# Performance work log

Measured on AMD Instinct MI355X. Metric: run time of the kernel, lower is better.

The kernel has to match this reference:

```python
import jax, jax.numpy as jnp
import numpy as np

N, D, E, T, R, KMEM, DE = 50000, 128, 800000, 400000, 1, 32, 16
EPS = 1e-5
BETA_MAX = 5.0
GRAD_CLIP = 1.0
STATE_CLIP = 10.0
STEP = 0.1
DAMP = 0.9999  # update_damping=1.0 clamped to 1-1e-4 as in __init__


def segment_logsumexp(s, idx, n):
    # numerically-stable per-segment logsumexp; empty segments contribute 0
    m = jax.ops.segment_max(s, idx, num_segments=n)
    ms = jnp.where(jnp.isfinite(m), m, 0.0)
    z = jax.ops.segment_sum(jnp.exp(s - ms[idx]), idx, num_segments=n)
    return jnp.where(z > 0, jnp.log(jnp.maximum(z, 1e-30)) + ms, 0.0)


def setup_inputs() -> dict:
    key = jax.random.key(0)
    ks = jax.random.split(key, 24)
    inv1 = jnp.log(jnp.expm1(jnp.float32(1.0)))  # _inv_softplus(1.0)
    xav = 0.5 * np.sqrt(2.0 / (2 * D))  # xavier_uniform gain=0.5 ~ std
    inp = {
        'X': jax.random.normal(ks[0], (N, D), jnp.float32),
        'edge_attr': jax.random.normal(ks[1], (E, DE), jnp.float32),
        'ln_gamma': jnp.ones((D,), jnp.float32),
        'ln_beta': jnp.zeros((D,), jnp.float32),
        'W_Q2': jax.random.normal(ks[2], (D, D), jnp.float32) * xav,
        'W_K2': jax.random.normal(ks[3], (D, D), jnp.float32) * xav,
        'W_Q3': jax.random.normal(ks[4], (D, R * D), jnp.float32) * xav,
        'W_K3': jax.random.normal(ks[5], (D, R * D), jnp.float32) * xav,
        'T_tau': jax.random.normal(ks[6], (2, R, D), jnp.float32) * 0.02,
        'W_Qm': jax.random.normal(ks[7], (D, D), jnp.float32) * xav,
        'W_Km': jax.random.normal(ks[8], (D, D), jnp.float32) * xav,
        'B_mem': jax.random.normal(ks[9], (KMEM, D), jnp.float32) / np.sqrt(D),
        'We1': jax.random.normal(ks[10], (DE, D), jnp.float32) / np.sqrt(DE),
        'be1': jnp.zeros((D,), jnp.float32),
        'We2': jax.random.normal(ks[11], (D, 1), jnp.float32) / np.sqrt(D),
        'be2': jnp.zeros((1,), jnp.float32),
        'lambda_2': inv1, 'lambda_3': inv1, 'lambda_m': inv1,
        'beta_2': inv1, 'beta_3': inv1, 'beta_m': inv1,
        'c_2': jax.random.randint(ks[12], (E,), 0, N),
        'u_2': jax.random.randint(ks[13], (E,), 0, N),
        'c_3': jax.random.randint(ks[14], (T,), 0, N),
        'u_3': jax.random.randint(ks[15], (T,), 0, N),
        'v_3': jax.random.randint(ks[16], (T,), 0, N),
        't_tau': jax.random.randint(ks[17], (T,), 0, 2),
    }
    return inp


def reference(X, edge_attr, ln_gamma, ln_beta, W_Q2, W_K2, W_Q3, W_K3, T_tau,
              W_Qm, W_Km, B_mem, We1, be1, We2, be2,
              lambda_2, lambda_3, lambda_m, beta_2, beta_3, beta_m,
              c_2, u_2, c_3, u_3, v_3, t_tau):
    sqrt_d = jnp.sqrt(jnp.float32(D))

    def energy(Xv):
        mu = jnp.mean(Xv, axis=-1, keepdims=True)
        var = jnp.var(Xv, axis=-1, keepdims=True)
        G = (Xv - mu) * jax.lax.rsqrt(var + EPS) * ln_gamma + ln_beta
        # pairwise (order-2) energy over edge list
        b2 = jnp.minimum(jax.nn.softplus(beta_2), BETA_MAX)
        Q2, K2 = G @ W_Q2, G @ W_K2
        a2 = (jax.nn.gelu(edge_attr @ We1 + be1) @ We2 + be2)[:, 0]  # edge_mlp bias
        s2 = b2 * (jnp.sum(Q2[c_2] * K2[u_2], axis=-1) / sqrt_d) + a2  # [E]
        E2 = -(jax.nn.softplus(lambda_2) / b2) * jnp.sum(segment_logsumexp(s2, c_2, N))
        # triplet (order-3) energy with per-type tensor T_tau
        b3 = jnp.minimum(jax.nn.softplus(beta_3), BETA_MAX)
        Q3 = (G @ W_Q3).reshape(-1, R, D)
        K3 = (G @ W_K3).reshape(-1, R, D)
        s3 = b3 * jnp.einsum('erd,erd,erd,erd->e', Q3[c_3], K3[u_3], K3[v_3],
                             T_tau[t_tau]) / jnp.float32(D)  # [T]
        E3 = -(jax.nn.softplus(lambda_3) / b3) * jnp.sum(segment_logsumexp(s3, c_3, N))
        # memory-bank energy
        bm = jnp.minimum(jax.nn.softplus(beta_m), BETA_MAX)
        sm = bm * ((G @ W_Qm) @ (B_mem @ W_Km).T) / sqrt_d  # [N,K]
        Em = -(jax.nn.softplus(lambda_m) / bm) * jnp.sum(jax.nn.logsumexp(sm, axis=1))
        return E2 + E3 + Em

    Eval, gX = jax.value_and_grad(energy)(X)
    gn = jnp.maximum(jnp.linalg.norm(gX, axis=-1, keepdims=True), 1e-6)
    gX = gX * jnp.minimum(GRAD_CLIP / gn, 1.0)
    X_next = X - STEP * DAMP * gX
    sn = jnp.maximum(jnp.linalg.norm(X_next, axis=-1, keepdims=True), 1e-6)
    X_next = X_next * jnp.minimum(STATE_CLIP / sn, 1.0)
    return (X_next, Eval)
```

## Files before the change

kernel.cpp:

```cpp
#include <hip/hip_runtime.h>

#define NN 50000
#define DD 128
#define EE 800000
#define TT 400000
#define KM 32
#define UU 320
#define SCAN_TILE 2048
#define SCAN_NB ((NN + SCAN_TILE - 1) / SCAN_TILE)

static constexpr float INV_SQRT_D = 0.08838834764831845f;
static constexpr float INV_D = 1.f / 128.f;

typedef __attribute__((ext_vector_type(8))) short bf16x8;
typedef __attribute__((ext_vector_type(4))) float f32x4;
typedef unsigned short ushort_t;

__device__ __forceinline__ float softplus_f(float x) {
  return (x > 20.f) ? x : log1pf(__expf(x));
}

__device__ __forceinline__ float gelu_fast(float x) {
  float p = fmaf(0.044715f * x * x, x, x);
  float e = __expf(-1.5957691216057308f * p);
  return x * __builtin_amdgcn_rcpf(1.f + e);
}

__device__ __forceinline__ float wredsum(float v) {
#pragma unroll
  for (int m = 32; m; m >>= 1) v += __shfl_xor(v, m, 64);
  return v;
}

__device__ __forceinline__ float redsum16(float v) {
#pragma unroll
  for (int m = 1; m < 16; m <<= 1) v += __shfl_xor(v, m, 64);
  return v;
}

__device__ __forceinline__ float blo(unsigned w) { return __uint_as_float(w << 16); }
__device__ __forceinline__ float bhi(unsigned w) { return __uint_as_float(w & 0xffff0000u); }
__device__ __forceinline__ unsigned pack_bf16(float a, float b) {
  unsigned ua = __float_as_uint(a); ua += 0x7fff + ((ua >> 16) & 1);
  unsigned ub = __float_as_uint(b); ub += 0x7fff + ((ub >> 16) & 1);
  return (ua >> 16) | (ub & 0xffff0000u);
}
__device__ __forceinline__ ushort_t bf16_1(float x) {
  unsigned u = __float_as_uint(x); u += 0x7fff + ((u >> 16) & 1);
  return (ushort_t)(u >> 16);
}
__device__ __forceinline__ void unp8(uint4 w, float* f) {
  f[0] = blo(w.x); f[1] = bhi(w.x); f[2] = blo(w.y); f[3] = bhi(w.y);
  f[4] = blo(w.z); f[5] = bhi(w.z); f[6] = blo(w.w); f[7] = bhi(w.w);
}
__device__ __forceinline__ uint4 pk8(const float* f) {
  uint4 r;
  r.x = pack_bf16(f[0], f[1]); r.y = pack_bf16(f[2], f[3]);
  r.z = pack_bf16(f[4], f[5]); r.w = pack_bf16(f[6], f[7]);
  return r;
}

__global__ void params_k(const float* l2, const float* l3, const float* lm,
                         const float* b2, const float* b3, const float* bm,
                         float* __restrict__ P) {
  if (threadIdx.x != 0) return;
  float B2 = fminf(softplus_f(b2[0]), 5.f);
  float B3 = fminf(softplus_f(b3[0]), 5.f);
  float Bm = fminf(softplus_f(bm[0]), 5.f);
  float S2 = softplus_f(l2[0]);
  float S3 = softplus_f(l3[0]);
  float Sm = softplus_f(lm[0]);
  P[0] = B2; P[1] = B3; P[2] = Bm;
  P[3] = -S2 * INV_SQRT_D; P[4] = -S3 * INV_D; P[5] = -Sm * INV_SQRT_D;
  P[6] = -S2 / B2; P[7] = -S3 / B3; P[8] = -Sm / Bm;
}

__global__ __launch_bounds__(256) void ln_fwd(const float* __restrict__ X,
                                              const float* __restrict__ gamma,
                                              const float* __restrict__ beta,
                                              unsigned* __restrict__ Gb,
                                              float* __restrict__ meanv,
                                              float* __restrict__ rstdv) {
  int row = blockIdx.x * 4 + (threadIdx.x >> 6);
  if (row >= NN) return;
  int l = threadIdx.x & 63;
  float2 x2 = *(const float2*)(X + row * DD + 2 * l);
  float mu = wredsum(x2.x + x2.y) * (1.f / DD);
  float d0 = x2.x - mu, d1 = x2.y - mu;
  float var = wredsum(d0 * d0 + d1 * d1) * (1.f / DD);
  float rstd = rsqrtf(var + 1e-5f);
  float2 g2 = *(const float2*)(gamma + 2 * l);
  float2 b2 = *(const float2*)(beta + 2 * l);
  float o0 = d0 * rstd * g2.x + b2.x;
  float o1 = d1 * rstd * g2.y + b2.y;
  Gb[(size_t)row * 64 + l] = pack_bf16(o0, o1);
  if (l == 0) { meanv[row] = mu; rstdv[row] = rstd; }
}

__global__ __launch_bounds__(256) void w_conv(const float* W0, const float* W1, const float* W2,
                                              const float* W3, const float* W4,
                                              ushort_t* __restrict__ Wt,
                                              ushort_t* __restrict__ Wc) {
  int idx = blockIdx.x * 256 + threadIdx.x;
  if (idx >= 640 * 128) return;
  const float* Ws[5] = {W0, W1, W2, W3, W4};
  int n = idx >> 7, k = idx & 127;
  Wt[idx] = bf16_1(Ws[n >> 7][(size_t)k * 128 + (n & 127)]);
  int k2 = idx >> 7, n2 = idx & 127;
  Wc[(size_t)n2 * 640 + k2] = bf16_1(Ws[k2 >> 7][(size_t)n2 * 128 + (k2 & 127)]);
}

__global__ __launch_bounds__(256) void mfma_fwd(const ushort_t* __restrict__ Gb,
                                                const ushort_t* __restrict__ Wt,
                                                ushort_t* __restrict__ QK, int M) {
  __shared__ ushort_t sB[64][136];
  int tid = threadIdx.x;
  int nb = blockIdx.y * 64;
  for (int idx = tid; idx < 64 * 16; idx += 256) {
    int r = idx >> 4, c8 = idx & 15;
    *(bf16x8*)&sB[r][c8 * 8] = *(const bf16x8*)(Wt + (size_t)(nb + r) * 128 + c8 * 8);
  }
  __syncthreads();
  int w = tid >> 6, l = tid & 63, quad = l >> 4, j = l & 15;
  int row0 = blockIdx.x * 64 + w * 16;
  int arow = row0 + j; if (arow >= M) arow = M - 1;
  const bf16x8* ap = (const bf16x8*)(Gb + (size_t)arow * 128);
  f32x4 acc[4];
#pragma unroll
  for (int nt = 0; nt < 4; nt++) acc[nt] = (f32x4){0.f, 0.f, 0.f, 0.f};
#pragma unroll
  for (int kc = 0; kc < 4; kc++) {
    bf16x8 a = ap[kc * 4 + quad];
#pragma unroll
    for (int nt = 0; nt < 4; nt++) {
      bf16x8 b = *(const bf16x8*)&sB[nt * 16 + j][kc * 32 + quad * 8];
      acc[nt] = __builtin_amdgcn_mfma_f32_16x16x32_bf16(a, b, acc[nt], 0, 0, 0);
    }
  }
#pragma unroll
  for (int nt = 0; nt < 4; nt++)
#pragma unroll
    for (int r = 0; r < 4; r++) {
      int row = row0 + quad * 4 + r;
      if (row < M) QK[(size_t)row * 640 + nb + nt * 16 + j] = bf16_1(acc[nt][r]);
    }
}

__global__ __launch_bounds__(256) void mfma_bwd(const ushort_t* __restrict__ dAll,
                                                const ushort_t* __restrict__ Wc,
                                                unsigned* __restrict__ dG, int M) {
  __shared__ ushort_t sB[64][40];
  int tid = threadIdx.x;
  int nb = blockIdx.y * 64;
  int w = tid >> 6, l = tid & 63, quad = l >> 4, j = l & 15;
  int row0 = blockIdx.x * 64 + w * 16;
  int arow = row0 + j; if (arow >= M) arow = M - 1;
  const ushort_t* arp = dAll + (size_t)arow * 640;
  f32x4 acc[4];
#pragma unroll
  for (int nt = 0; nt < 4; nt++) acc[nt] = (f32x4){0.f, 0.f, 0.f, 0.f};
  int sr = tid >> 2, sc = tid & 3;
  for (int kc = 0; kc < 20; kc++) {
    __syncthreads();
    *(bf16x8*)&sB[sr][sc * 8] = *(const bf16x8*)(Wc + (size_t)(nb + sr) * 640 + kc * 32 + sc * 8);
    __syncthreads();
    bf16x8 a = *(const bf16x8*)(arp + kc * 32 + quad * 8);
#pragma unroll
    for (int nt = 0; nt < 4; nt++) {
      bf16x8 b = *(const bf16x8*)&sB[nt * 16 + j][quad * 8];
      acc[nt] = __builtin_amdgcn_mfma_f32_16x16x32_bf16(a, b, acc[nt], 0, 0, 0);
    }
  }
#pragma unroll
  for (int nt = 0; nt < 4; nt++)
#pragma unroll
    for (int r = 0; r < 4; r++) {
      int row = row0 + quad * 4 + r;
      if (row < M) ((ushort_t*)dG)[(size_t)row * 128 + nb + nt * 16 + j] = bf16_1(acc[nt][r]);
    }
}

__global__ __launch_bounds__(256, 1) void gemm_km(const float* __restrict__ A,
                                                  const float* __restrict__ W,
                                                  float* __restrict__ C, int M) {
  __shared__ float As[32][132];
  __shared__ float Wst[128][136];
  const int tid = threadIdx.x;
  for (int idx = tid; idx < 128 * 128; idx += 256) {
    int k = idx >> 7, jj = idx & 127;
    Wst[k][jj] = W[k * 128 + jj];
  }
  for (int idx = tid; idx < 32 * 128; idx += 256) {
    int r = idx >> 7, d = idx & 127;
    As[r][d] = A[r * 128 + d];
  }
  __syncthreads();
  int r = tid >> 3, c0 = (tid & 7) * 16;
  float acc[16];
#pragma unroll
  for (int q = 0; q < 16; q++) acc[q] = 0.f;
  for (int k = 0; k < 128; k++) {
    float av = As[r][k];
#pragma unroll
    for (int q = 0; q < 16; q++) acc[q] = fmaf(av, Wst[k][c0 + q], acc[q]);
  }
#pragma unroll
  for (int q = 0; q < 16; q++) C[r * 128 + c0 + q] = acc[q];
}

__global__ __launch_bounds__(256) void edge_mlp(const float* __restrict__ EA,
                                                const float* __restrict__ We1,
                                                const float* __restrict__ be1,
                                                const float* __restrict__ We2,
                                                const float* __restrict__ be2,
                                                float* __restrict__ a2) {
  __shared__ float sW1[16 * 128];
  __shared__ float sb1[128];
  __shared__ float sW2[128];
  int tid = threadIdx.x;
  for (int i = tid; i < 2048; i += 256) sW1[i] = We1[i];
  if (tid < 128) { sb1[tid] = be1[tid]; sW2[tid] = We2[tid]; }
  __syncthreads();
  int w = tid >> 6, l = tid & 63;
  int m = l & 15, q = l >> 4;
  union u8 { bf16x8 v; ushort_t s[8]; };
  u8 bf[8];
  float bb[8], ww[8];
#pragma unroll
  for (int nt = 0; nt < 8; nt++) {
    int n = nt * 16 + m;
#pragma unroll
    for (int j = 0; j < 8; j++) {
      int k = q * 8 + j;
      bf[nt].s[j] = (k < 16) ? bf16_1(sW1[k * 128 + n]) : (ushort_t)0;
    }
    bb[nt] = sb1[n];
    ww[nt] = sW2[n];
  }
  float be2v = be2[0];
  for (int batch = 0; batch < 4; batch++) {
    int e0 = blockIdx.x * 256 + batch * 64 + w * 16;
    u8 af;
    if (q < 2) {
      const float* ep = EA + (size_t)(e0 + m) * 16 + q * 8;
      float4 v0 = *(const float4*)ep;
      float4 v1 = *(const float4*)(ep + 4);
      af.s[0] = bf16_1(v0.x); af.s[1] = bf16_1(v0.y);
      af.s[2] = bf16_1(v0.z); af.s[3] = bf16_1(v0.w);
      af.s[4] = bf16_1(v1.x); af.s[5] = bf16_1(v1.y);
      af.s[6] = bf16_1(v1.z); af.s[7] = bf16_1(v1.w);
    } else {
#pragma unroll
      for (int j = 0; j < 8; j++) af.s[j] = 0;
    }
    float s0 = 0.f, s1 = 0.f, s2 = 0.f, s3 = 0.f;
#pragma unroll
    for (int nt = 0; nt < 8; nt++) {
      float bias = bb[nt];
      f32x4 cin = (f32x4){bias, bias, bias, bias};
      f32x4 acc = __builtin_amdgcn_mfma_f32_16x16x32_bf16(af.v, bf[nt].v, cin, 0, 0, 0);
      float w2v = ww[nt];
      s0 = fmaf(gelu_fast(acc[0]), w2v, s0);
      s1 = fmaf(gelu_fast(acc[1]), w2v, s1);
      s2 = fmaf(gelu_fast(acc[2]), w2v, s2);
      s3 = fmaf(gelu_fast(acc[3]), w2v, s3);
    }
    s0 = redsum16(s0); s1 = redsum16(s1); s2 = redsum16(s2); s3 = redsum16(s3);
    if (m == 0) {
      int eb = e0 + q * 4;
      a2[eb + 0] = s0 + be2v;
      a2[eb + 1] = s1 + be2v;
      a2[eb + 2] = s2 + be2v;
      a2[eb + 3] = s3 + be2v;
    }
  }
}

__global__ __launch_bounds__(256) void hist2(const int* __restrict__ a,
                                             const int* __restrict__ b,
                                             int* __restrict__ ca,
                                             int* __restrict__ cb, int n) {
  int base = blockIdx.x * 2048 + threadIdx.x;
  if (base + 1792 < n) {
    int av[8], bv[8];
#pragma unroll
    for (int k = 0; k < 8; k++) { int e = base + k * 256; av[k] = a[e]; bv[k] = b[e]; }
#pragma unroll
    for (int k = 0; k < 8; k++) atomicAdd(&ca[av[k]], 1);
#pragma unroll
    for (int k = 0; k < 8; k++) atomicAdd(&cb[bv[k]], 1);
  } else {
#pragma unroll
    for (int k = 0; k < 8; k++) {
      int e = base + k * 256;
      if (e < n) { atomicAdd(&ca[a[e]], 1); atomicAdd(&cb[b[e]], 1); }
    }
  }
}

__global__ __launch_bounds__(256) void hist_t3(const int* __restrict__ c,
                                               const int* __restrict__ u,
                                               const int* __restrict__ v,
                                               int* __restrict__ cc,
                                               int* __restrict__ cuv, int n) {
  int base = blockIdx.x * 2048 + threadIdx.x;
  if (base + 1792 < n) {
    int cv[8], uv[8], vv[8];
#pragma unroll
    for (int k = 0; k < 8; k++) { int t = base + k * 256; cv[k] = c[t]; uv[k] = u[t]; vv[k] = v[t]; }
#pragma unroll
    for (int k = 0; k < 8; k++) atomicAdd(&cc[cv[k]], 1);
#pragma unroll
    for (int k = 0; k < 8; k++) atomicAdd(&cuv[uv[k]], 1);
#pragma unroll
    for (int k = 0; k < 8; k++) atomicAdd(&cuv[vv[k]], 1);
  } else {
#pragma unroll
    for (int k = 0; k < 8; k++) {
      int t = base + k * 256;
      if (t < n) { atomicAdd(&cc[c[t]], 1); atomicAdd(&cuv[u[t]], 1); atomicAdd(&cuv[v[t]], 1); }
    }
  }
}

__global__ __launch_bounds__(256) void scan_p1(const int* __restrict__ cnt,
                                               int* __restrict__ part) {
  int arr = blockIdx.y, b = blockIdx.x;
  const int* c = cnt + (size_t)arr * NN;
  int gi = b * SCAN_TILE + threadIdx.x * 8;
  int s = 0;
#pragma unroll
  for (int t = 0; t < 8; t++) s += (gi + t < NN) ? c[gi + t] : 0;
#pragma unroll
  for (int m = 32; m; m >>= 1) s += __shfl_xor(s, m, 64);
  __shared__ int wt[4];
  int lane = threadIdx.x & 63, wid = threadIdx.x >> 6;
  if (lane == 0) wt[wid] = s;
  __syncthreads();
  if (threadIdx.x == 0) part[arr * SCAN_NB + b] = wt[0] + wt[1] + wt[2] + wt[3];
}

__global__ __launch_bounds__(256) void scan_p2(int* __restrict__ part) {
  int w = threadIdx.x >> 6, l = threadIdx.x & 63;
  int v = (l < SCAN_NB) ? part[w * SCAN_NB + l] : 0;
  int x = v;
#pragma unroll
  for (int d = 1; d < 64; d <<= 1) {
    int y = __shfl_up(x, d, 64);
    if (l >= d) x += y;
  }
  if (l < SCAN_NB) part[w * SCAN_NB + l] = x - v;
}

__global__ __launch_bounds__(256) void scan_p3(const int* __restrict__ cnt,
                                               const int* __restrict__ part,
                                               int* __restrict__ rowptr,
                                               int* __restrict__ cursor) {
  int arr = blockIdx.y, b = blockIdx.x;
  const int* c = cnt + (size_t)arr * NN;
  int* rp = rowptr + (size_t)arr * (NN + 1);
  int* cur = cursor + (size_t)arr * NN;
  int tid = threadIdx.x;
  int gi = b * SCAN_TILE + tid * 8;
  int vals[8];
#pragma unroll
  for (int t = 0; t < 8; t++) vals[t] = (gi + t < NN) ? c[gi + t] : 0;
  int tsum = 0;
#pragma unroll
  for (int t = 0; t < 8; t++) tsum += vals[t];
  int lane = tid & 63, wid = tid >> 6;
  int x = tsum;
#pragma unroll
  for (int d = 1; d < 64; d <<= 1) {
    int y = __shfl_up(x, d, 64);
    if (lane >= d) x += y;
  }
  __shared__ int wt[4];
  if (lane == 63) wt[wid] = x;
  __syncthreads();
  int wadd = 0;
  for (int w = 0; w < wid; w++) wadd += wt[w];
  int running = part[arr * SCAN_NB + b] + wadd + x - tsum;
#pragma unroll
  for (int t = 0; t < 8; t++) {
    if (gi + t < NN) { rp[gi + t] = running; cur[gi + t] = running; }
    running += vals[t];
  }
  if (b == SCAN_NB - 1 && tid == 255) rp[NN] = running;
}

__global__ __launch_bounds__(256) void scat2(const int* __restrict__ c2,
                                             const int* __restrict__ u2,
                                             const float* __restrict__ a2,
                                             int* __restrict__ cuc,
                                             int* __restrict__ cuu,
                                             uint2* __restrict__ payc,
                                             uint2* __restrict__ payu, int n) {
  int base = blockIdx.x * 2048 + threadIdx.x;
  if (base + 1792 < n) {
    int c[8], u[8]; float a[8]; int p[8], p2[8];
#pragma unroll
    for (int k = 0; k < 8; k++) { int e = base + k * 256; c[k] = c2[e]; u[k] = u2[e]; a[k] = a2[e]; }
#pragma unroll
    for (int k = 0; k < 8; k++) p[k] = atomicAdd(&cuc[c[k]], 1);
#pragma unroll
    for (int k = 0; k < 8; k++) p2[k] = atomicAdd(&cuu[u[k]], 1);
#pragma unroll
    for (int k = 0; k < 8; k++) {
      uint2 t; t.x = (unsigned)u[k]; t.y = __float_as_uint(a[k]);
      payc[p[k]] = t;
    }
#pragma unroll
    for (int k = 0; k < 8; k++) {
      uint2 t; t.x = (unsigned)p[k]; t.y = (unsigned)c[k];
      payu[p2[k]] = t;
    }
  } else {
#pragma unroll
    for (int k = 0; k < 8; k++) {
      int e = base + k * 256;
      if (e < n) {
        int cc = c2[e], uu = u2[e];
        int pp = atomicAdd(&cuc[cc], 1);
        int qq = atomicAdd(&cuu[uu], 1);
        uint2 t; t.x = (unsigned)uu; t.y = __float_as_uint(a2[e]);
        payc[pp] = t;
        uint2 t2; t2.x = (unsigned)pp; t2.y = (unsigned)cc;
        payu[qq] = t2;
      }
    }
  }
}

__global__ __launch_bounds__(256) void scat_t3(const int* __restrict__ c3,
                                               const int* __restrict__ u3,
                                               const int* __restrict__ v3,
                                               const int* __restrict__ ttau,
                                               int* __restrict__ cuc,
                                               int* __restrict__ cuv,
                                               uint2* __restrict__ payc,
                                               uint2* __restrict__ payuv, int n) {
  int base = blockIdx.x * 1024 + threadIdx.x;
  if (base + 768 < n) {
    int c[4], u[4], v[4], ta[4]; int p[4], q1[4], q2[4];
#pragma unroll
    for (int k = 0; k < 4; k++) {
      int t = base + k * 256;
      c[k] = c3[t]; u[k] = u3[t]; v[k] = v3[t]; ta[k] = ttau[t] & 1;
    }
#pragma unroll
    for (int k = 0; k < 4; k++) p[k] = atomicAdd(&cuc[c[k]], 1);
#pragma unroll
    for (int k = 0; k < 4; k++) q1[k] = atomicAdd(&cuv[u[k]], 1);
#pragma unroll
    for (int k = 0; k < 4; k++) q2[k] = atomicAdd(&cuv[v[k]], 1);
#pragma unroll
    for (int k = 0; k < 4; k++) {
      uint2 a; a.x = ((unsigned)u[k] << 16) | (unsigned)v[k]; a.y = (unsigned)ta[k];
      payc[p[k]] = a;
    }
#pragma unroll
    for (int k = 0; k < 4; k++) {
      unsigned sp = ((unsigned)p[k] << 1) | (unsigned)ta[k];
      uint2 b1; b1.x = ((unsigned)v[k] << 16) | (unsigned)c[k]; b1.y = sp;
      payuv[q1[k]] = b1;
      uint2 b2; b2.x = ((unsigned)u[k] << 16) | (unsigned)c[k]; b2.y = sp;
      payuv[q2[k]] = b2;
    }
  } else {
#pragma unroll
    for (int k = 0; k < 4; k++) {
      int t = base + k * 256;
      if (t < n) {
        int c = c3[t], u = u3[t], v = v3[t], ta = ttau[t] & 1;
        int p = atomicAdd(&cuc[c], 1);
        int q1 = atomicAdd(&cuv[u], 1);
        int q2 = atomicAdd(&cuv[v], 1);
        unsigned sp = ((unsigned)p << 1) | (unsigned)ta;
        uint2 a; a.x = ((unsigned)u << 16) | (unsigned)v; a.y = (unsigned)ta;
        payc[p] = a;
        uint2 b1; b1.x = ((unsigned)v << 16) | (unsigned)c; b1.y = sp;
        payuv[q1] = b1;
        uint2 b2; b2.x = ((unsigned)u << 16) | (unsigned)c; b2.y = sp;
        payuv[q2] = b2;
      }
    }
  }
}

__global__ __launch_bounds__(256) void e2_fused(const unsigned* __restrict__ QK,
                                                const float* __restrict__ P,
                                                const uint2* __restrict__ pay,
                                                const int* __restrict__ rp,
                                                float* __restrict__ s2c,
                                                float* __restrict__ L2,
                                                unsigned* __restrict__ dAll) {
  int row = blockIdx.x * 4 + (threadIdx.x >> 6);
  if (row >= NN) return;
  int l = threadIdx.x & 63, g = l >> 4, j = l & 15;
  float b2s = P[0] * INV_SQRT_D, cw2 = P[3];
  float q[8];
  unp8(*(const uint4*)(QK + (size_t)row * UU + j * 4), q);
  int s = rp[row], e = rp[row + 1];
  float m = -3.0e38f, z = 0.f;
  float acc[8] = {0.f, 0.f, 0.f, 0.f, 0.f, 0.f, 0.f, 0.f};
  int i0 = s + g;
  uint4 kA = {0, 0, 0, 0}, kB = {0, 0, 0, 0};
  float aA = 0.f, aB = 0.f;
  if (i0 < e) {
    uint2 w = pay[i0]; aA = __uint_as_float(w.y);
    kA = *(const uint4*)(QK + (size_t)w.x * UU + 64 + j * 4);
  }
  if (i0 + 4 < e) {
    uint2 w = pay[i0 + 4]; aB = __uint_as_float(w.y);
    kB = *(const uint4*)(QK + (size_t)w.x * UU + 64 + j * 4);
  }
  for (int i = i0; i < e; i += 4) {
    uint4 kC = {0, 0, 0, 0}; float aC = 0.f;
    if (i + 8 < e) {
      uint2 w = pay[i + 8]; aC = __uint_as_float(w.y);
      kC = *(const uint4*)(QK + (size_t)w.x * UU + 64 + j * 4);
    }
    float k[8]; unp8(kA, k);
    float d = 0.f;
#pragma unroll
    for (int t = 0; t < 8; t++) d = fmaf(q[t], k[t], d);
    d = redsum16(d);
    float sv = b2s * d + aA;
    if (j == 0) s2c[i] = sv;
    if (sv <= m) {
      float p = __expf(sv - m);
      z += p;
#pragma unroll
      for (int t = 0; t < 8; t++) acc[t] = fmaf(p, k[t], acc[t]);
    } else {
      float r = __expf(m - sv);
      z = fmaf(z, r, 1.f);
#pragma unroll
      for (int t = 0; t < 8; t++) acc[t] = fmaf(acc[t], r, k[t]);
      m = sv;
    }
    kA = kB; aA = aB; kB = kC; aB = aC;
  }
  float mx = fmaxf(m, __shfl_xor(m, 16, 64));
  mx = fmaxf(mx, __shfl_xor(mx, 32, 64));
  float r = (z > 0.f) ? __expf(m - mx) : 0.f;
  float zz = z * r;
  zz += __shfl_xor(zz, 16, 64);
  zz += __shfl_xor(zz, 32, 64);
#pragma unroll
  for (int t = 0; t < 8; t++) {
    float v = acc[t] * r;
    v += __shfl_xor(v, 16, 64);
    v += __shfl_xor(v, 32, 64);
    acc[t] = v;
  }
  if (l == 0) L2[row] = (zz > 0.f) ? (mx + __logf(zz)) : 0.f;
  if (g == 0) {
    float coef = (zz > 0.f) ? cw2 / zz : 0.f;
    float o[8];
#pragma unroll
    for (int t = 0; t < 8; t++) o[t] = coef * acc[t];
    *(uint4*)(dAll + (size_t)row * UU + 0 + j * 4) = pk8(o);
  }
}

__global__ __launch_bounds__(256) void dk2_gather(const unsigned* __restrict__ QK,
                                                  const float* __restrict__ s2c,
                                                  const float* __restrict__ L2,
                                                  const float* __restrict__ P,
                                                  const uint2* __restrict__ pay,
                                                  const int* __restrict__ rp,
                                                  unsigned* __restrict__ dAll) {
  int row = blockIdx.x * 4 + (threadIdx.x >> 6);
  if (row >= NN) return;
  int l = threadIdx.x & 63, g = l >> 4, j = l & 15;
  float cw2 = P[3];
  int s = rp[row], e = rp[row + 1];
  float acc[8] = {0.f, 0.f, 0.f, 0.f, 0.f, 0.f, 0.f, 0.f};
  int i0 = s + g;
  uint4 qA = {0, 0, 0, 0}, qB = {0, 0, 0, 0};
  float scA = 0.f, lcA = 0.f, scB = 0.f, lcB = 0.f;
  if (i0 < e) {
    uint2 w = pay[i0]; scA = s2c[w.x]; lcA = L2[w.y];
    qA = *(const uint4*)(QK + (size_t)w.y * UU + 0 + j * 4);
  }
  if (i0 + 4 < e) {
    uint2 w = pay[i0 + 4]; scB = s2c[w.x]; lcB = L2[w.y];
    qB = *(const uint4*)(QK + (size_t)w.y * UU + 0 + j * 4);
  }
  for (int i = i0; i < e; i += 4) {
    uint4 qC = {0, 0, 0, 0}; float scC = 0.f, lcC = 0.f;
    if (i + 8 < e) {
      uint2 w = pay[i + 8]; scC = s2c[w.x]; lcC = L2[w.y];
      qC = *(const uint4*)(QK + (size_t)w.y * UU + 0 + j * 4);
    }
    float w = cw2 * __expf(scA - lcA);
    float qv[8]; unp8(qA, qv);
#pragma unroll
    for (int t = 0; t < 8; t++) acc[t] = fmaf(w, qv[t], acc[t]);
    qA = qB; scA = scB; lcA = lcB;
    qB = qC; scB = scC; lcB = lcC;
  }
#pragma unroll
  for (int t = 0; t < 8; t++) {
    float v = acc[t];
    v += __shfl_xor(v, 16, 64);
    v += __shfl_xor(v, 32, 64);
    acc[t] = v;
  }
  if (g == 0) *(uint4*)(dAll + (size_t)row * UU + 64 + j * 4) = pk8(acc);
}

__global__ __launch_bounds__(256) void t3_fused(const unsigned* __restrict__ QK,
                                                const float* __restrict__ Tt,
                                                const float* __restrict__ P,
                                                const uint2* __restrict__ pay,
                                                const int* __restrict__ rp,
                                                float* __restrict__ s3c,
                                                float* __restrict__ L3,
                                                unsigned* __restrict__ dAll) {
  __shared__ float sT[2 * DD];
  int tid = threadIdx.x;
  sT[tid] = Tt[tid];
  __syncthreads();
  int row = blockIdx.x * 4 + (tid >> 6);
  if (row >= NN) return;
  int l = tid & 63, g = l >> 4, j = l & 15;
  float b3s = P[1] * INV_D, cw3 = P[4];
  float q[8];
  unp8(*(const uint4*)(QK + (size_t)row * UU + 128 + j * 4), q);
  int s = rp[row], e = rp[row + 1];
  float m = -3.0e38f, z = 0.f;
  float acc[8] = {0.f, 0.f, 0.f, 0.f, 0.f, 0.f, 0.f, 0.f};
  int i0 = s + g;
  uint4 kuA = {0, 0, 0, 0}, kvA = {0, 0, 0, 0};
  uint4 kuB = {0, 0, 0, 0}, kvB = {0, 0, 0, 0};
  int taA = 0, taB = 0;
  if (i0 < e) {
    uint2 w = pay[i0]; int u = w.x >> 16, v = w.x & 0xffff; taA = (int)w.y;
    kuA = *(const uint4*)(QK + (size_t)u * UU + 192 + j * 4);
    kvA = *(const uint4*)(QK + (size_t)v * UU + 192 + j * 4);
  }
  if (i0 + 4 < e) {
    uint2 w = pay[i0 + 4]; int u = w.x >> 16, v = w.x & 0xffff; taB = (int)w.y;
    kuB = *(const uint4*)(QK + (size_t)u * UU + 192 + j * 4);
    kvB = *(const uint4*)(QK + (size_t)v * UU + 192 + j * 4);
  }
  for (int i = i0; i < e; i += 4) {
    uint4 kuC = {0, 0, 0, 0}, kvC = {0, 0, 0, 0}; int taC = 0;
    if (i + 8 < e) {
      uint2 w = pay[i + 8]; int u = w.x >> 16, v = w.x & 0xffff; taC = (int)w.y;
      kuC = *(const uint4*)(QK + (size_t)u * UU + 192 + j * 4);
      kvC = *(const uint4*)(QK + (size_t)v * UU + 192 + j * 4);
    }
    float ku[8], kv[8]; unp8(kuA, ku); unp8(kvA, kv);
    const float* tv = &sT[taA * DD + j * 8];
    float et[8], d = 0.f;
#pragma unroll
    for (int t = 0; t < 8; t++) { et[t] = ku[t] * kv[t] * tv[t]; d = fmaf(q[t], et[t], d); }
    d = redsum16(d);
    float sv = b3s * d;
    if (j == 0) s3c[i] = sv;
    if (sv <= m) {
      float p = __expf(sv - m);
      z += p;
#pragma unroll
      for (int t = 0; t < 8; t++) acc[t] = fmaf(p, et[t], acc[t]);
    } else {
      float r = __expf(m - sv);
      z = fmaf(z, r, 1.f);
#pragma unroll
      for (int t = 0; t < 8; t++) acc[t] = fmaf(acc[t], r, et[t]);
      m = sv;
    }
    kuA = kuB; kvA = kvB; taA = taB;
    kuB = kuC; kvB = kvC; taB = taC;
  }
  float mx = fmaxf(m, __shfl_xor(m, 16, 64));
  mx = fmaxf(mx, __shfl_xor(mx, 32, 64));
  float r = (z > 0.f) ? __expf(m - mx) : 0.f;
  float zz = z * r;
  zz += __shfl_xor(zz, 16, 64);
  zz += __shfl_xor(zz, 32, 64);
#pragma unroll
  for (int t = 0; t < 8; t++) {
    float v = acc[t] * r;
    v += __shfl_xor(v, 16, 64);
    v += __shfl_xor(v, 32, 64);
    acc[t] = v;
  }
  if (l == 0) L3[row] = (zz > 0.f) ? (mx + __logf(zz)) : 0.f;
  if (g == 0) {
    float coef = (zz > 0.f) ? cw3 / zz : 0.f;
    float o[8];
#pragma unroll
    for (int t = 0; t < 8; t++) o[t] = coef * acc[t];
    *(uint4*)(dAll + (size_t)row * UU + 128 + j * 4) = pk8(o);
  }
}

__global__ __launch_bounds__(256) void dk3_gather(const unsigned* __restrict__ QK,
                                                  const float* __restrict__ Tt,
                                                  const float* __restrict__ s3c,
                                                  const float* __restrict__ L3,
                                                  const float* __restrict__ P,
                                                  const uint2* __restrict__ pay,
                                                  const int* __restrict__ rp,
                                                  unsigned* __restrict__ dAll) {
  __shared__ float sT[2 * DD];
  int tid = threadIdx.x;
  sT[tid] = Tt[tid];
  __syncthreads();
  int row = blockIdx.x * 4 + (tid >> 6);
  if (row >= NN) return;
  int l = tid & 63, g = l >> 4, j = l & 15;
  float cw3 = P[4];
  int s = rp[row], e = rp[row + 1];
  float acc[8] = {0.f, 0.f, 0.f, 0.f, 0.f, 0.f, 0.f, 0.f};
  int i0 = s + g;
  uint4 qA = {0, 0, 0, 0}, kA = {0, 0, 0, 0};
  uint4 qB = {0, 0, 0, 0}, kB = {0, 0, 0, 0};
  int taA = 0, taB = 0;
  float scA = 0.f, lcA = 0.f, scB = 0.f, lcB = 0.f;
  if (i0 < e) {
    uint2 w = pay[i0]; int o = w.x >> 16, c = w.x & 0xffff; unsigned sp = w.y;
    taA = (int)(sp & 1); scA = s3c[sp >> 1]; lcA = L3[c];
    qA = *(const uint4*)(QK + (size_t)c * UU + 128 + j * 4);
    kA = *(const uint4*)(QK + (size_t)o * UU + 192 + j * 4);
  }
  if (i0 + 4 < e) {
    uint2 w = pay[i0 + 4]; int o = w.x >> 16, c = w.x & 0xffff; unsigned sp = w.y;
    taB = (int)(sp & 1); scB = s3c[sp >> 1]; lcB = L3[c];
    qB = *(const uint4*)(QK + (size_t)c * UU + 128 + j * 4);
    kB = *(const uint4*)(QK + (size_t)o * UU + 192 + j * 4);
  }
  for (int i = i0; i < e; i += 4) {
    uint4 qC = {0, 0, 0, 0}, kC = {0, 0, 0, 0}; int taC = 0;
    float scC = 0.f, lcC = 0.f;
    if (i + 8 < e) {
      uint2 w = pay[i + 8]; int o = w.x >> 16, c = w.x & 0xffff; unsigned sp = w.y;
      taC = (int)(sp & 1); scC = s3c[sp >> 1]; lcC = L3[c];
      qC = *(const uint4*)(QK + (size_t)c * UU + 128 + j * 4);
      kC = *(const uint4*)(QK + (size_t)o * UU + 192 + j * 4);
    }
    float w = cw3 * __expf(scA - lcA);
    float qv[8], ko[8]; unp8(qA, qv); unp8(kA, ko);
    const float* tv = &sT[taA * DD + j * 8];
#pragma unroll
    for (int t = 0; t < 8; t++) acc[t] = fmaf(w * tv[t], qv[t] * ko[t], acc[t]);
    qA = qB; kA = kB; taA = taB; scA = scB; lcA = lcB;
    qB = qC; kB = kC; taB = taC; scB = scC; lcB = lcC;
  }
#pragma unroll
  for (int t = 0; t < 8; t++) {
    float v = acc[t];
    v += __shfl_xor(v, 16, 64);
    v += __shfl_xor(v, 32, 64);
    acc[t] = v;
  }
  if (g == 0) *(uint4*)(dAll + (size_t)row * UU + 192 + j * 4) = pk8(acc);
}

__global__ __launch_bounds__(256) void em_row(const unsigned* __restrict__ QK,
                                              const float* __restrict__ Km,
                                              const float* __restrict__ P,
                                              unsigned* __restrict__ dAll,
                                              float* __restrict__ Lm) {
  __shared__ float sKm[KM * DD];
  int tid = threadIdx.x;
  for (int i = tid; i < KM * DD; i += 256) sKm[i] = Km[i];
  __syncthreads();
  int row = blockIdx.x * 4 + (tid >> 6);
  if (row >= NN) return;
  int l = tid & 63, g = l >> 4, j = l & 15;
  float bms = P[2] * INV_SQRT_D, cwm = P[5];
  float q[8];
  unp8(*(const uint4*)(QK + (size_t)row * UU + 256 + j * 4), q);
  float dk[8];
#pragma unroll
  for (int kk = 0; kk < 8; kk++) {
    int k = g * 8 + kk;
    const float* kr = &sKm[k * DD + j * 8];
    float d = 0.f;
#pragma unroll
    for (int t = 0; t < 8; t++) d = fmaf(q[t], kr[t], d);
    dk[kk] = redsum16(d) * bms;
  }
  float m = dk[0];
#pragma unroll
  for (int kk = 1; kk < 8; kk++) m = fmaxf(m, dk[kk]);
  float mx = fmaxf(m, __shfl_xor(m, 16, 64));
  mx = fmaxf(mx, __shfl_xor(mx, 32, 64));
  float p[8], z = 0.f;
#pragma unroll
  for (int kk = 0; kk < 8; kk++) { p[kk] = __expf(dk[kk] - mx); z += p[kk]; }
  float zz = z;
  zz += __shfl_xor(zz, 16, 64);
  zz += __shfl_xor(zz, 32, 64);
  if (l == 0) Lm[row] = mx + __logf(zz);
  float coef = cwm / zz;
  float acc[8] = {0.f, 0.f, 0.f, 0.f, 0.f, 0.f, 0.f, 0.f};
#pragma unroll
  for (int kk = 0; kk < 8; kk++) {
    int k = g * 8 + kk;
    const float* kr = &sKm[k * DD + j * 8];
    float pc_ = p[kk] * coef;
#pragma unroll
    for (int t = 0; t < 8; t++) acc[t] = fmaf(pc_, kr[t], acc[t]);
  }
#pragma unroll
  for (int t = 0; t < 8; t++) {
    float v = acc[t];
    v += __shfl_xor(v, 16, 64);
    v += __shfl_xor(v, 32, 64);
    acc[t] = v;
  }
  if (g == 0) *(uint4*)(dAll + (size_t)row * UU + 256 + j * 4) = pk8(acc);
}

__global__ __launch_bounds__(256) void ln_bwd(const float* __restrict__ X,
                                              const unsigned* __restrict__ dG,
                                              const float* __restrict__ gamma,
                                              const float* __restrict__ meanv,
                                              const float* __restrict__ rstdv,
                                              float* __restrict__ out) {
  int row = blockIdx.x * 4 + (threadIdx.x >> 6);
  if (row >= NN) return;
  int l = threadIdx.x & 63;
  float mu = meanv[row], rstd = rstdv[row];
  float2 x2 = *(const float2*)(X + row * DD + 2 * l);
  unsigned gw = dG[(size_t)row * 64 + l];
  float2 ga = *(const float2*)(gamma + 2 * l);
  float xh0 = (x2.x - mu) * rstd, xh1 = (x2.y - mu) * rstd;
  float dh0 = blo(gw) * ga.x, dh1 = bhi(gw) * ga.y;
  float sa = wredsum(dh0 + dh1) * (1.f / DD);
  float sb = wredsum(dh0 * xh0 + dh1 * xh1) * (1.f / DD);
  float dx0 = rstd * (dh0 - sa - xh0 * sb);
  float dx1 = rstd * (dh1 - sa - xh1 * sb);
  float gn = fmaxf(sqrtf(wredsum(dx0 * dx0 + dx1 * dx1)), 1e-6f);
  float sc = fminf(1.f / gn, 1.f);
  dx0 *= sc; dx1 *= sc;
  float xn0 = x2.x - 0.1f * 0.9999f * dx0;
  float xn1 = x2.y - 0.1f * 0.9999f * dx1;
  float sn = fmaxf(sqrtf(wredsum(xn0 * xn0 + xn1 * xn1)), 1e-6f);
  float sc2 = fminf(10.f / sn, 1.f);
  float2 o; o.x = xn0 * sc2; o.y = xn1 * sc2;
  *(float2*)(out + row * DD + 2 * l) = o;
}

__global__ __launch_bounds__(256) void eval_write(const float* __restrict__ L2,
                                                  const float* __restrict__ L3,
                                                  const float* __restrict__ Lm,
                                                  const float* __restrict__ P,
                                                  float* __restrict__ out) {
  int i = blockIdx.x * 256 + threadIdx.x;
  float a2 = 0.f, a3 = 0.f, am = 0.f;
  if (i < NN) { a2 = L2[i]; a3 = L3[i]; am = Lm[i]; }
  a2 = wredsum(a2); a3 = wredsum(a3); am = wredsum(am);
  __shared__ float r2[4], r3[4], rm[4];
  int wv = threadIdx.x >> 6, l = threadIdx.x & 63;
  if (l == 0) { r2[wv] = a2; r3[wv] = a3; rm[wv] = am; }
  __syncthreads();
  if (threadIdx.x == 0) {
    float S2 = r2[0] + r2[1] + r2[2] + r2[3];
    float S3 = r3[0] + r3[1] + r3[2] + r3[3];
    float Sm = rm[0] + rm[1] + rm[2] + rm[3];
    atomicAdd(out, P[6] * S2 + P[7] * S3 + P[8] * Sm);
  }
}

extern "C" void kernel_launch(void* const* d_in, const int* in_sizes, int n_in,
                              void* d_out, int out_size, void* d_ws, size_t ws_size,
                              hipStream_t stream) {
  (void)in_sizes; (void)n_in; (void)out_size;
  const float* X = (const float*)d_in[0];
  const float* EA = (const float*)d_in[1];
  const float* ln_g = (const float*)d_in[2];
  const float* ln_b = (const float*)d_in[3];
  const float* W_Q2 = (const float*)d_in[4];
  const float* W_K2 = (const float*)d_in[5];
  const float* W_Q3 = (const float*)d_in[6];
  const float* W_K3 = (const float*)d_in[7];
  const float* T_tau = (const float*)d_in[8];
  const float* W_Qm = (const float*)d_in[9];
  const float* W_Km = (const float*)d_in[10];
  const float* B_mem = (const float*)d_in[11];
  const float* We1 = (const float*)d_in[12];
  const float* be1 = (const float*)d_in[13];
  const float* We2 = (const float*)d_in[14];
  const float* be2 = (const float*)d_in[15];
  const float* l2s = (const float*)d_in[16];
  const float* l3s = (const float*)d_in[17];
  const float* lms = (const float*)d_in[18];
  const float* b2s = (const float*)d_in[19];
  const float* b3s = (const float*)d_in[20];
  const float* bms = (const float*)d_in[21];
  const int* c2 = (const int*)d_in[22];
  const int* u2 = (const int*)d_in[23];
  const int* c3 = (const int*)d_in[24];
  const int* u3 = (const int*)d_in[25];
  const int* v3 = (const int*)d_in[26];
  const int* ttau = (const int*)d_in[27];
  float* out = (float*)d_out;

  float* ws = (float*)d_ws;
  size_t off = 0;
  auto alloc = [&](size_t n) { float* p = ws + off; off += n; return p; };
  const size_t ND = (size_t)NN * DD;
  unsigned* Gb = (unsigned*)alloc(ND / 2);
  unsigned* QKall = (unsigned*)alloc((size_t)NN * UU);
  unsigned* dAll = (unsigned*)alloc((size_t)NN * UU);
  unsigned* dG = (unsigned*)alloc(ND / 2);
  ushort_t* Wt5 = (ushort_t*)alloc(640 * 128 / 2);
  ushort_t* Wcat = (ushort_t*)alloc(640 * 128 / 2);
  float* Km = alloc((size_t)KM * DD);
  float* a2 = alloc(EE);
  float* s2c = alloc(EE);
  float* s3c = alloc(TT);
  float* meanv = alloc(NN);
  float* rstdv = alloc(NN);
  float* L2 = alloc(NN);
  float* L3 = alloc(NN);
  float* Lm = alloc(NN);
  float* Pparams = alloc(16);
  int* cnt = (int*)alloc(4 * (size_t)NN);
  int* rowptr = (int*)alloc(4 * (size_t)(NN + 1));
  int* cursor = (int*)alloc(4 * (size_t)NN);
  int* spart = (int*)alloc(4 * SCAN_NB);
  uint2* payc2 = (uint2*)alloc(2 * (size_t)EE);
  uint2* payu2 = (uint2*)alloc(2 * (size_t)EE);
  uint2* payc3 = (uint2*)alloc(2 * (size_t)TT);
  uint2* payuv = (uint2*)alloc(4 * (size_t)TT);
  if (off * sizeof(float) > ws_size) return;

  int* cnt_c2 = cnt, *cnt_u2 = cnt + NN, *cnt_c3 = cnt + 2 * NN, *cnt_uv = cnt + 3 * NN;
  int* rp_c2 = rowptr, *rp_u2 = rowptr + (NN + 1), *rp_c3 = rowptr + 2 * (NN + 1), *rp_uv = rowptr + 3 * (NN + 1);
  int* cu_c2 = cursor, *cu_u2 = cursor + NN, *cu_c3 = cursor + 2 * NN, *cu_uv = cursor + 3 * NN;

  hipMemsetAsync(cnt, 0, 4ull * NN * sizeof(int), stream);
  hipMemsetAsync(out + ND, 0, sizeof(float), stream);

  params_k<<<1, 64, 0, stream>>>(l2s, l3s, lms, b2s, b3s, bms, Pparams);

  int rowB = (NN + 3) / 4;
  int mB = (NN + 63) / 64;

  ln_fwd<<<rowB, 256, 0, stream>>>(X, ln_g, ln_b, Gb, meanv, rstdv);
  w_conv<<<320, 256, 0, stream>>>(W_Q2, W_K2, W_Q3, W_K3, W_Qm, Wt5, Wcat);
  mfma_fwd<<<dim3(mB, 10), 256, 0, stream>>>((const ushort_t*)Gb, Wt5, (ushort_t*)QKall, NN);
  gemm_km<<<1, 256, 0, stream>>>(B_mem, W_Km, Km, KM);
  edge_mlp<<<EE / 256, 256, 0, stream>>>(EA, We1, be1, We2, be2, a2);

  hist2<<<(EE + 2047) / 2048, 256, 0, stream>>>(c2, u2, cnt_c2, cnt_u2, EE);
  hist_t3<<<(TT + 2047) / 2048, 256, 0, stream>>>(c3, u3, v3, cnt_c3, cnt_uv, TT);
  scan_p1<<<dim3(SCAN_NB, 4), 256, 0, stream>>>(cnt, spart);
  scan_p2<<<1, 256, 0, stream>>>(spart);
  scan_p3<<<dim3(SCAN_NB, 4), 256, 0, stream>>>(cnt, spart, rowptr, cursor);
  scat2<<<(EE + 2047) / 2048, 256, 0, stream>>>(c2, u2, a2, cu_c2, cu_u2, payc2, payu2, EE);
  scat_t3<<<(TT + 1023) / 1024, 256, 0, stream>>>(c3, u3, v3, ttau, cu_c3, cu_uv,
                                                  payc3, payuv, TT);

  e2_fused<<<rowB, 256, 0, stream>>>(QKall, Pparams, payc2, rp_c2, s2c, L2, dAll);
  dk2_gather<<<rowB, 256, 0, stream>>>(QKall, s2c, L2, Pparams, payu2, rp_u2, dAll);
  t3_fused<<<rowB, 256, 0, stream>>>(QKall, T_tau, Pparams, payc3, rp_c3, s3c, L3, dAll);
  dk3_gather<<<rowB, 256, 0, stream>>>(QKall, T_tau, s3c, L3, Pparams, payuv, rp_uv, dAll);
  em_row<<<rowB, 256, 0, stream>>>(QKall, Km, Pparams, dAll, Lm);

  mfma_bwd<<<dim3(mB, 2), 256, 0, stream>>>((const ushort_t*)dAll, Wcat, dG, NN);

  ln_bwd<<<rowB, 256, 0, stream>>>(X, dG, ln_g, meanv, rstdv, out);
  eval_write<<<(NN + 255) / 256, 256, 0, stream>>>(L2, L3, Lm, Pparams, out + ND);
}
```

Measured before the change: 861.6 us.

## Merge independent kernels into combined launches with block-range dispatch

Independent kernels are folded into single launches that split work by block index: the forward MFMA projection with the edge MLP, the two histograms, the two scatters, the e2/t3/memory-bank row kernels, and the two dk gathers. Histogram and scatter blocks now process 1024 elements instead of 2048, giving more blocks. The aim is to cut launch overhead and tail idle time by letting independent work overlap on the GPU. In exchange, shared memory is sized for the largest branch, register pressure is the maximum over branches, and blocks in one launch can be unevenly loaded.

```diff
diff --git a/kernel.cpp b/kernel.cpp
--- a/kernel.cpp
+++ b/kernel.cpp
@@ -6,6 +6,11 @@
 #define TT 400000
 #define KM 32
 #define UU 320
+#define ROWB 12500
+#define MB 782
+#define EDGE_BLKS 3125
+#define HB2 782
+#define HBT 391
 #define SCAN_TILE 2048
 #define SCAN_NB ((NN + SCAN_TILE - 1) / SCAN_TILE)
 
@@ -110,19 +115,19 @@
   Wc[(size_t)n2 * 640 + k2] = bf16_1(Ws[k2 >> 7][(size_t)n2 * 128 + (k2 & 127)]);
 }
 
-__global__ __launch_bounds__(256) void mfma_fwd(const ushort_t* __restrict__ Gb,
-                                                const ushort_t* __restrict__ Wt,
-                                                ushort_t* __restrict__ QK, int M) {
+__device__ void mfma_fwd_body(int bxr, int by, const ushort_t* __restrict__ Gb,
+                              const ushort_t* __restrict__ Wt,
+                              ushort_t* __restrict__ QK, int M) {
   __shared__ ushort_t sB[64][136];
   int tid = threadIdx.x;
-  int nb = blockIdx.y * 64;
+  int nb = by * 64;
   for (int idx = tid; idx < 64 * 16; idx += 256) {
     int r = idx >> 4, c8 = idx & 15;
     *(bf16x8*)&sB[r][c8 * 8] = *(const bf16x8*)(Wt + (size_t)(nb + r) * 128 + c8 * 8);
   }
   __syncthreads();
   int w = tid >> 6, l = tid & 63, quad = l >> 4, j = l & 15;
-  int row0 = blockIdx.x * 64 + w * 16;
+  int row0 = bxr * 64 + w * 16;
   int arow = row0 + j; if (arow >= M) arow = M - 1;
   const bf16x8* ap = (const bf16x8*)(Gb + (size_t)arow * 128);
   f32x4 acc[4];
@@ -146,74 +151,12 @@
     }
 }
 
-__global__ __launch_bounds__(256) void mfma_bwd(const ushort_t* __restrict__ dAll,
-                                                const ushort_t* __restrict__ Wc,
-                                                unsigned* __restrict__ dG, int M) {
-  __shared__ ushort_t sB[64][40];
-  int tid = threadIdx.x;
-  int nb = blockIdx.y * 64;
-  int w = tid >> 6, l = tid & 63, quad = l >> 4, j = l & 15;
-  int row0 = blockIdx.x * 64 + w * 16;
-  int arow = row0 + j; if (arow >= M) arow = M - 1;
-  const ushort_t* arp = dAll + (size_t)arow * 640;
-  f32x4 acc[4];
-#pragma unroll
-  for (int nt = 0; nt < 4; nt++) acc[nt] = (f32x4){0.f, 0.f, 0.f, 0.f};
-  int sr = tid >> 2, sc = tid & 3;
-  for (int kc = 0; kc < 20; kc++) {
-    __syncthreads();
-    *(bf16x8*)&sB[sr][sc * 8] = *(const bf16x8*)(Wc + (size_t)(nb + sr) * 640 + kc * 32 + sc * 8);
-    __syncthreads();
-    bf16x8 a = *(const bf16x8*)(arp + kc * 32 + quad * 8);
-#pragma unroll
-    for (int nt = 0; nt < 4; nt++) {
-      bf16x8 b = *(const bf16x8*)&sB[nt * 16 + j][quad * 8];
-      acc[nt] = __builtin_amdgcn_mfma_f32_16x16x32_bf16(a, b, acc[nt], 0, 0, 0);
-    }
-  }
-#pragma unroll
-  for (int nt = 0; nt < 4; nt++)
-#pragma unroll
-    for (int r = 0; r < 4; r++) {
-      int row = row0 + quad * 4 + r;
-      if (row < M) ((ushort_t*)dG)[(size_t)row * 128 + nb + nt * 16 + j] = bf16_1(acc[nt][r]);
-    }
-}
-
-__global__ __launch_bounds__(256, 1) void gemm_km(const float* __restrict__ A,
-                                                  const float* __restrict__ W,
-                                                  float* __restrict__ C, int M) {
-  __shared__ float As[32][132];
-  __shared__ float Wst[128][136];
-  const int tid = threadIdx.x;
-  for (int idx = tid; idx < 128 * 128; idx += 256) {
-    int k = idx >> 7, jj = idx & 127;
-    Wst[k][jj] = W[k * 128 + jj];
-  }
-  for (int idx = tid; idx < 32 * 128; idx += 256) {
-    int r = idx >> 7, d = idx & 127;
-    As[r][d] = A[r * 128 + d];
-  }
-  __syncthreads();
-  int r = tid >> 3, c0 = (tid & 7) * 16;
-  float acc[16];
-#pragma unroll
-  for (int q = 0; q < 16; q++) acc[q] = 0.f;
-  for (int k = 0; k < 128; k++) {
-    float av = As[r][k];
-#pragma unroll
-    for (int q = 0; q < 16; q++) acc[q] = fmaf(av, Wst[k][c0 + q], acc[q]);
-  }
-#pragma unroll
-  for (int q = 0; q < 16; q++) C[r * 128 + c0 + q] = acc[q];
-}
-
-__global__ __launch_bounds__(256) void edge_mlp(const float* __restrict__ EA,
-                                                const float* __restrict__ We1,
-                                                const float* __restrict__ be1,
-                                                const float* __restrict__ We2,
-                                                const float* __restrict__ be2,
-                                                float* __restrict__ a2) {
+__device__ void edge_mlp_body(int bx, const float* __restrict__ EA,
+                              const float* __restrict__ We1,
+                              const float* __restrict__ be1,
+                              const float* __restrict__ We2,
+                              const float* __restrict__ be2,
+                              float* __restrict__ a2) {
   __shared__ float sW1[16 * 128];
   __shared__ float sb1[128];
   __shared__ float sW2[128];
@@ -239,7 +182,7 @@
   }
   float be2v = be2[0];
   for (int batch = 0; batch < 4; batch++) {
-    int e0 = blockIdx.x * 256 + batch * 64 + w * 16;
+    int e0 = bx * 256 + batch * 64 + w * 16;
     u8 af;
     if (q < 2) {
       const float* ep = EA + (size_t)(e0 + m) * 16 + q * 8;
@@ -276,51 +219,142 @@
   }
 }
 
-__global__ __launch_bounds__(256) void hist2(const int* __restrict__ a,
-                                             const int* __restrict__ b,
-                                             int* __restrict__ ca,
-                                             int* __restrict__ cb, int n) {
-  int base = blockIdx.x * 2048 + threadIdx.x;
-  if (base + 1792 < n) {
-    int av[8], bv[8];
-#pragma unroll
-    for (int k = 0; k < 8; k++) { int e = base + k * 256; av[k] = a[e]; bv[k] = b[e]; }
-#pragma unroll
-    for (int k = 0; k < 8; k++) atomicAdd(&ca[av[k]], 1);
-#pragma unroll
-    for (int k = 0; k < 8; k++) atomicAdd(&cb[bv[k]], 1);
+__global__ __launch_bounds__(256) void fwd_k(const ushort_t* __restrict__ Gb,
+                                             const ushort_t* __restrict__ Wt,
+                                             ushort_t* __restrict__ QK,
+                                             const float* __restrict__ EA,
+                                             const float* __restrict__ We1,
+                                             const float* __restrict__ be1,
+                                             const float* __restrict__ We2,
+                                             const float* __restrict__ be2,
+                                             float* __restrict__ a2) {
+  int bx = blockIdx.x;
+  if (bx < MB * 10) {
+    mfma_fwd_body(bx / 10, bx % 10, Gb, Wt, QK, NN);
   } else {
-#pragma unroll
-    for (int k = 0; k < 8; k++) {
+    edge_mlp_body(bx - MB * 10, EA, We1, be1, We2, be2, a2);
+  }
+}
+
+__global__ __launch_bounds__(256) void mfma_bwd(const ushort_t* __restrict__ dAll,
+                                                const ushort_t* __restrict__ Wc,
+                                                unsigned* __restrict__ dG, int M) {
+  __shared__ ushort_t sB[64][40];
+  int tid = threadIdx.x;
+  int nb = blockIdx.y * 64;
+  int w = tid >> 6, l = tid & 63, quad = l >> 4, j = l & 15;
+  int row0 = blockIdx.x * 64 + w * 16;
+  int arow = row0 + j; if (arow >= M) arow = M - 1;
+  const ushort_t* arp = dAll + (size_t)arow * 640;
+  f32x4 acc[4];
+#pragma unroll
+  for (int nt = 0; nt < 4; nt++) acc[nt] = (f32x4){0.f, 0.f, 0.f, 0.f};
+  int sr = tid >> 2, sc = tid & 3;
+  for (int kc = 0; kc < 20; kc++) {
+    __syncthreads();
+    *(bf16x8*)&sB[sr][sc * 8] = *(const bf16x8*)(Wc + (size_t)(nb + sr) * 640 + kc * 32 + sc * 8);
+    __syncthreads();
+    bf16x8 a = *(const bf16x8*)(arp + kc * 32 + quad * 8);
+#pragma unroll
+    for (int nt = 0; nt < 4; nt++) {
+      bf16x8 b = *(const bf16x8*)&sB[nt * 16 + j][quad * 8];
+      acc[nt] = __builtin_amdgcn_mfma_f32_16x16x32_bf16(a, b, acc[nt], 0, 0, 0);
+    }
+  }
+#pragma unroll
+  for (int nt = 0; nt < 4; nt++)
+#pragma unroll
+    for (int r = 0; r < 4; r++) {
+      int row = row0 + quad * 4 + r;
+      if (row < M) ((ushort_t*)dG)[(size_t)row * 128 + nb + nt * 16 + j] = bf16_1(acc[nt][r]);
+    }
+}
+
+__global__ __launch_bounds__(256, 1) void gemm_km(const float* __restrict__ A,
+                                                  const float* __restrict__ W,
+                                                  float* __restrict__ C, int M) {
+  __shared__ float As[32][132];
+  __shared__ float Wst[128][136];
+  const int tid = threadIdx.x;
+  for (int idx = tid; idx < 128 * 128; idx += 256) {
+    int k = idx >> 7, jj = idx & 127;
+    Wst[k][jj] = W[k * 128 + jj];
+  }
+  for (int idx = tid; idx < 32 * 128; idx += 256) {
+    int r = idx >> 7, d = idx & 127;
+    As[r][d] = A[r * 128 + d];
+  }
+  __syncthreads();
+  int r = tid >> 3, c0 = (tid & 7) * 16;
+  float acc[16];
+#pragma unroll
+  for (int q = 0; q < 16; q++) acc[q] = 0.f;
+  for (int k = 0; k < 128; k++) {
+    float av = As[r][k];
+#pragma unroll
+    for (int q = 0; q < 16; q++) acc[q] = fmaf(av, Wst[k][c0 + q], acc[q]);
+  }
+#pragma unroll
+  for (int q = 0; q < 16; q++) C[r * 128 + c0 + q] = acc[q];
+}
+
+__device__ void hist2_body(int bx, const int* __restrict__ a,
+                           const int* __restrict__ b,
+                           int* __restrict__ ca, int* __restrict__ cb, int n) {
+  int base = bx * 1024 + threadIdx.x;
+  if (base + 768 < n) {
+    int av[4], bv[4];
+#pragma unroll
+    for (int k = 0; k < 4; k++) { int e = base + k * 256; av[k] = a[e]; bv[k] = b[e]; }
+#pragma unroll
+    for (int k = 0; k < 4; k++) atomicAdd(&ca[av[k]], 1);
+#pragma unroll
+    for (int k = 0; k < 4; k++) atomicAdd(&cb[bv[k]], 1);
+  } else {
+#pragma unroll
+    for (int k = 0; k < 4; k++) {
       int e = base + k * 256;
       if (e < n) { atomicAdd(&ca[a[e]], 1); atomicAdd(&cb[b[e]], 1); }
     }
   }
 }
 
-__global__ __launch_bounds__(256) void hist_t3(const int* __restrict__ c,
-                                               const int* __restrict__ u,
-                                               const int* __restrict__ v,
-                                               int* __restrict__ cc,
-                                               int* __restrict__ cuv, int n) {
-  int base = blockIdx.x * 2048 + threadIdx.x;
-  if (base + 1792 < n) {
-    int cv[8], uv[8], vv[8];
-#pragma unroll
-    for (int k = 0; k < 8; k++) { int t = base + k * 256; cv[k] = c[t]; uv[k] = u[t]; vv[k] = v[t]; }
-#pragma unroll
-    for (int k = 0; k < 8; k++) atomicAdd(&cc[cv[k]], 1);
-#pragma unroll
-    for (int k = 0; k < 8; k++) atomicAdd(&cuv[uv[k]], 1);
-#pragma unroll
-    for (int k = 0; k < 8; k++) atomicAdd(&cuv[vv[k]], 1);
+__device__ void hist_t3_body(int bx, const int* __restrict__ c,
+                             const int* __restrict__ u,
+                             const int* __restrict__ v,
+                             int* __restrict__ cc, int* __restrict__ cuv, int n) {
+  int base = bx * 1024 + threadIdx.x;
+  if (base + 768 < n) {
+    int cv[4], uv[4], vv[4];
+#pragma unroll
+    for (int k = 0; k < 4; k++) { int t = base + k * 256; cv[k] = c[t]; uv[k] = u[t]; vv[k] = v[t]; }
+#pragma unroll
+    for (int k = 0; k < 4; k++) atomicAdd(&cc[cv[k]], 1);
+#pragma unroll
+    for (int k = 0; k < 4; k++) atomicAdd(&cuv[uv[k]], 1);
+#pragma unroll
+    for (int k = 0; k < 4; k++) atomicAdd(&cuv[vv[k]], 1);
   } else {
 #pragma unroll
-    for (int k = 0; k < 8; k++) {
+    for (int k = 0; k < 4; k++) {
       int t = base + k * 256;
       if (t < n) { atomicAdd(&cc[c[t]], 1); atomicAdd(&cuv[u[t]], 1); atomicAdd(&cuv[v[t]], 1); }
     }
   }
+}
+
+__global__ __launch_bounds__(256) void hist_k(const int* __restrict__ c2,
+                                              const int* __restrict__ u2,
+                                              const int* __restrict__ c3,
+                                              const int* __restrict__ u3,
+                                              const int* __restrict__ v3,
+                                              int* __restrict__ cnt_c2,
+                                              int* __restrict__ cnt_u2,
+                                              int* __restrict__ cnt_c3,
+                                              int* __restrict__ cnt_uv) {
+  int bx = blockIdx.x;
+  if (bx < HB2) hist2_body(bx, c2, u2, cnt_c2, cnt_u2, EE);
+  else hist_t3_body(bx - HB2, c3, u3, v3, cnt_c3, cnt_uv, TT);
 }
 
 __global__ __launch_bounds__(256) void scan_p1(const int* __restrict__ cnt,
@@ -389,35 +423,33 @@
   if (b == SCAN_NB - 1 && tid == 255) rp[NN] = running;
 }
 
-__global__ __launch_bounds__(256) void scat2(const int* __restrict__ c2,
-                                             const int* __restrict__ u2,
-                                             const float* __restrict__ a2,
-                                             int* __restrict__ cuc,
-                                             int* __restrict__ cuu,
-                                             uint2* __restrict__ payc,
-                                             uint2* __restrict__ payu, int n) {
-  int base = blockIdx.x * 2048 + threadIdx.x;
-  if (base + 1792 < n) {
-    int c[8], u[8]; float a[8]; int p[8], p2[8];
-#pragma unroll
-    for (int k = 0; k < 8; k++) { int e = base + k * 256; c[k] = c2[e]; u[k] = u2[e]; a[k] = a2[e]; }
-#pragma unroll
-    for (int k = 0; k < 8; k++) p[k] = atomicAdd(&cuc[c[k]], 1);
-#pragma unroll
-    for (int k = 0; k < 8; k++) p2[k] = atomicAdd(&cuu[u[k]], 1);
-#pragma unroll
-    for (int k = 0; k < 8; k++) {
+__device__ void scat2_body(int bx, const int* __restrict__ c2,
+                           const int* __restrict__ u2,
+                           const float* __restrict__ a2,
+                           int* __restrict__ cuc, int* __restrict__ cuu,
+                           uint2* __restrict__ payc, uint2* __restrict__ payu, int n) {
+  int base = bx * 1024 + threadIdx.x;
+  if (base + 768 < n) {
+    int c[4], u[4]; float a[4]; int p[4], p2[4];
+#pragma unroll
+    for (int k = 0; k < 4; k++) { int e = base + k * 256; c[k] = c2[e]; u[k] = u2[e]; a[k] = a2[e]; }
+#pragma unroll
+    for (int k = 0; k < 4; k++) p[k] = atomicAdd(&cuc[c[k]], 1);
+#pragma unroll
+    for (int k = 0; k < 4; k++) p2[k] = atomicAdd(&cuu[u[k]], 1);
+#pragma unroll
+    for (int k = 0; k < 4; k++) {
       uint2 t; t.x = (unsigned)u[k]; t.y = __float_as_uint(a[k]);
       payc[p[k]] = t;
     }
 #pragma unroll
-    for (int k = 0; k < 8; k++) {
+    for (int k = 0; k < 4; k++) {
       uint2 t; t.x = (unsigned)p[k]; t.y = (unsigned)c[k];
       payu[p2[k]] = t;
     }
   } else {
 #pragma unroll
-    for (int k = 0; k < 8; k++) {
+    for (int k = 0; k < 4; k++) {
       int e = base + k * 256;
       if (e < n) {
         int cc = c2[e], uu = u2[e];
@@ -432,15 +464,13 @@
   }
 }
 
-__global__ __launch_bounds__(256) void scat_t3(const int* __restrict__ c3,
-                                               const int* __restrict__ u3,
-                                               const int* __restrict__ v3,
-                                               const int* __restrict__ ttau,
-                                               int* __restrict__ cuc,
-                                               int* __restrict__ cuv,
-                                               uint2* __restrict__ payc,
-                                               uint2* __restrict__ payuv, int n) {
-  int base = blockIdx.x * 1024 + threadIdx.x;
+__device__ void scat_t3_body(int bx, const int* __restrict__ c3,
+                             const int* __restrict__ u3,
+                             const int* __restrict__ v3,
+                             const int* __restrict__ ttau,
+                             int* __restrict__ cuc, int* __restrict__ cuv,
+                             uint2* __restrict__ payc, uint2* __restrict__ payuv, int n) {
+  int base = bx * 1024 + threadIdx.x;
   if (base + 768 < n) {
     int c[4], u[4], v[4], ta[4]; int p[4], q1[4], q2[4];
 #pragma unroll
@@ -488,15 +518,34 @@
   }
 }
 
-__global__ __launch_bounds__(256) void e2_fused(const unsigned* __restrict__ QK,
-                                                const float* __restrict__ P,
-                                                const uint2* __restrict__ pay,
-                                                const int* __restrict__ rp,
-                                                float* __restrict__ s2c,
-                                                float* __restrict__ L2,
-                                                unsigned* __restrict__ dAll) {
-  int row = blockIdx.x * 4 + (threadIdx.x >> 6);
-  if (row >= NN) return;
+__global__ __launch_bounds__(256) void scat_k(const int* __restrict__ c2,
+                                              const int* __restrict__ u2,
+                                              const float* __restrict__ a2,
+                                              int* __restrict__ cu_c2,
+                                              int* __restrict__ cu_u2,
+                                              uint2* __restrict__ payc2,
+                                              uint2* __restrict__ payu2,
+                                              const int* __restrict__ c3,
+                                              const int* __restrict__ u3,
+                                              const int* __restrict__ v3,
+                                              const int* __restrict__ ttau,
+                                              int* __restrict__ cu_c3,
+                                              int* __restrict__ cu_uv,
+                                              uint2* __restrict__ payc3,
+                                              uint2* __restrict__ payuv) {
+  int bx = blockIdx.x;
+  if (bx < HB2) scat2_body(bx, c2, u2, a2, cu_c2, cu_u2, payc2, payu2, EE);
+  else scat_t3_body(bx - HB2, c3, u3, v3, ttau, cu_c3, cu_uv, payc3, payuv, TT);
+}
+
+__device__ void e2_body(int bx, const unsigned* __restrict__ QK,
+                        const float* __restrict__ P,
+                        const uint2* __restrict__ pay,
+                        const int* __restrict__ rp,
+                        float* __restrict__ s2c,
+                        float* __restrict__ L2,
+                        unsigned* __restrict__ dAll) {
+  int row = bx * 4 + (threadIdx.x >> 6);
   int l = threadIdx.x & 63, g = l >> 4, j = l & 15;
   float b2s = P[0] * INV_SQRT_D, cw2 = P[3];
   float q[8];
@@ -565,67 +614,19 @@
   }
 }
 
-__global__ __launch_bounds__(256) void dk2_gather(const unsigned* __restrict__ QK,
-                                                  const float* __restrict__ s2c,
-                                                  const float* __restrict__ L2,
-                                                  const float* __restrict__ P,
-                                                  const uint2* __restrict__ pay,
-                                                  const int* __restrict__ rp,
-                                                  unsigned* __restrict__ dAll) {
-  int row = blockIdx.x * 4 + (threadIdx.x >> 6);
-  if (row >= NN) return;
-  int l = threadIdx.x & 63, g = l >> 4, j = l & 15;
-  float cw2 = P[3];
-  int s = rp[row], e = rp[row + 1];
-  float acc[8] = {0.f, 0.f, 0.f, 0.f, 0.f, 0.f, 0.f, 0.f};
-  int i0 = s + g;
-  uint4 qA = {0, 0, 0, 0}, qB = {0, 0, 0, 0};
-  float scA = 0.f, lcA = 0.f, scB = 0.f, lcB = 0.f;
-  if (i0 < e) {
-    uint2 w = pay[i0]; scA = s2c[w.x]; lcA = L2[w.y];
-    qA = *(const uint4*)(QK + (size_t)w.y * UU + 0 + j * 4);
-  }
-  if (i0 + 4 < e) {
-    uint2 w = pay[i0 + 4]; scB = s2c[w.x]; lcB = L2[w.y];
-    qB = *(const uint4*)(QK + (size_t)w.y * UU + 0 + j * 4);
-  }
-  for (int i = i0; i < e; i += 4) {
-    uint4 qC = {0, 0, 0, 0}; float scC = 0.f, lcC = 0.f;
-    if (i + 8 < e) {
-      uint2 w = pay[i + 8]; scC = s2c[w.x]; lcC = L2[w.y];
-      qC = *(const uint4*)(QK + (size_t)w.y * UU + 0 + j * 4);
-    }
-    float w = cw2 * __expf(scA - lcA);
-    float qv[8]; unp8(qA, qv);
-#pragma unroll
-    for (int t = 0; t < 8; t++) acc[t] = fmaf(w, qv[t], acc[t]);
-    qA = qB; scA = scB; lcA = lcB;
-    qB = qC; scB = scC; lcB = lcC;
-  }
-#pragma unroll
-  for (int t = 0; t < 8; t++) {
-    float v = acc[t];
-    v += __shfl_xor(v, 16, 64);
-    v += __shfl_xor(v, 32, 64);
-    acc[t] = v;
-  }
-  if (g == 0) *(uint4*)(dAll + (size_t)row * UU + 64 + j * 4) = pk8(acc);
-}
-
-__global__ __launch_bounds__(256) void t3_fused(const unsigned* __restrict__ QK,
-                                                const float* __restrict__ Tt,
-                                                const float* __restrict__ P,
-                                                const uint2* __restrict__ pay,
-                                                const int* __restrict__ rp,
-                                                float* __restrict__ s3c,
-                                                float* __restrict__ L3,
-                                                unsigned* __restrict__ dAll) {
+__device__ void t3_body(int bx, const unsigned* __restrict__ QK,
+                        const float* __restrict__ Tt,
+                        const float* __restrict__ P,
+                        const uint2* __restrict__ pay,
+                        const int* __restrict__ rp,
+                        float* __restrict__ s3c,
+                        float* __restrict__ L3,
+                        unsigned* __restrict__ dAll) {
   __shared__ float sT[2 * DD];
   int tid = threadIdx.x;
   sT[tid] = Tt[tid];
   __syncthreads();
-  int row = blockIdx.x * 4 + (tid >> 6);
-  if (row >= NN) return;
+  int row = bx * 4 + (tid >> 6);
   int l = tid & 63, g = l >> 4, j = l & 15;
   float b3s = P[1] * INV_D, cw3 = P[4];
   float q[8];
@@ -700,20 +701,141 @@
   }
 }
 
-__global__ __launch_bounds__(256) void dk3_gather(const unsigned* __restrict__ QK,
-                                                  const float* __restrict__ Tt,
-                                                  const float* __restrict__ s3c,
-                                                  const float* __restrict__ L3,
-                                                  const float* __restrict__ P,
-                                                  const uint2* __restrict__ pay,
-                                                  const int* __restrict__ rp,
-                                                  unsigned* __restrict__ dAll) {
+__device__ void em_body(int bx, const unsigned* __restrict__ QK,
+                        const float* __restrict__ Km,
+                        const float* __restrict__ P,
+                        unsigned* __restrict__ dAll,
+                        float* __restrict__ Lm) {
+  __shared__ float sKm[KM * DD];
+  int tid = threadIdx.x;
+  for (int i = tid; i < KM * DD; i += 256) sKm[i] = Km[i];
+  __syncthreads();
+  int row = bx * 4 + (tid >> 6);
+  int l = tid & 63, g = l >> 4, j = l & 15;
+  float bms = P[2] * INV_SQRT_D, cwm = P[5];
+  float q[8];
+  unp8(*(const uint4*)(QK + (size_t)row * UU + 256 + j * 4), q);
+  float dk[8];
+#pragma unroll
+  for (int kk = 0; kk < 8; kk++) {
+    int k = g * 8 + kk;
+    const float* kr = &sKm[k * DD + j * 8];
+    float d = 0.f;
+#pragma unroll
+    for (int t = 0; t < 8; t++) d = fmaf(q[t], kr[t], d);
+    dk[kk] = redsum16(d) * bms;
+  }
+  float m = dk[0];
+#pragma unroll
+  for (int kk = 1; kk < 8; kk++) m = fmaxf(m, dk[kk]);
+  float mx = fmaxf(m, __shfl_xor(m, 16, 64));
+  mx = fmaxf(mx, __shfl_xor(mx, 32, 64));
+  float p[8], z = 0.f;
+#pragma unroll
+  for (int kk = 0; kk < 8; kk++) { p[kk] = __expf(dk[kk] - mx); z += p[kk]; }
+  float zz = z;
+  zz += __shfl_xor(zz, 16, 64);
+  zz += __shfl_xor(zz, 32, 64);
+  if (l == 0) Lm[row] = mx + __logf(zz);
+  float coef = cwm / zz;
+  float acc[8] = {0.f, 0.f, 0.f, 0.f, 0.f, 0.f, 0.f, 0.f};
+#pragma unroll
+  for (int kk = 0; kk < 8; kk++) {
+    int k = g * 8 + kk;
+    const float* kr = &sKm[k * DD + j * 8];
+    float pc_ = p[kk] * coef;
+#pragma unroll
+    for (int t = 0; t < 8; t++) acc[t] = fmaf(pc_, kr[t], acc[t]);
+  }
+#pragma unroll
+  for (int t = 0; t < 8; t++) {
+    float v = acc[t];
+    v += __shfl_xor(v, 16, 64);
+    v += __shfl_xor(v, 32, 64);
+    acc[t] = v;
+  }
+  if (g == 0) *(uint4*)(dAll + (size_t)row * UU + 256 + j * 4) = pk8(acc);
+}
+
+__global__ __launch_bounds__(256) void phase2_k(const unsigned* __restrict__ QK,
+                                                const float* __restrict__ Tt,
+                                                const float* __restrict__ Km,
+                                                const float* __restrict__ P,
+                                                const uint2* __restrict__ payc2,
+                                                const int* __restrict__ rp_c2,
+                                                const uint2* __restrict__ payc3,
+                                                const int* __restrict__ rp_c3,
+                                                float* __restrict__ s2c,
+                                                float* __restrict__ L2,
+                                                float* __restrict__ s3c,
+                                                float* __restrict__ L3,
+                                                float* __restrict__ Lm,
+                                                unsigned* __restrict__ dAll) {
+  int bx = blockIdx.x;
+  if (bx < ROWB) e2_body(bx, QK, P, payc2, rp_c2, s2c, L2, dAll);
+  else if (bx < 2 * ROWB) t3_body(bx - ROWB, QK, Tt, P, payc3, rp_c3, s3c, L3, dAll);
+  else em_body(bx - 2 * ROWB, QK, Km, P, dAll, Lm);
+}
+
+__device__ void dk2_body(int bx, const unsigned* __restrict__ QK,
+                         const float* __restrict__ s2c,
+                         const float* __restrict__ L2,
+                         const float* __restrict__ P,
+                         const uint2* __restrict__ pay,
+                         const int* __restrict__ rp,
+                         unsigned* __restrict__ dAll) {
+  int row = bx * 4 + (threadIdx.x >> 6);
+  int l = threadIdx.x & 63, g = l >> 4, j = l & 15;
+  float cw2 = P[3];
+  int s = rp[row], e = rp[row + 1];
+  float acc[8] = {0.f, 0.f, 0.f, 0.f, 0.f, 0.f, 0.f, 0.f};
+  int i0 = s + g;
+  uint4 qA = {0, 0, 0, 0}, qB = {0, 0, 0, 0};
+  float scA = 0.f, lcA = 0.f, scB = 0.f, lcB = 0.f;
+  if (i0 < e) {
+    uint2 w = pay[i0]; scA = s2c[w.x]; lcA = L2[w.y];
+    qA = *(const uint4*)(QK + (size_t)w.y * UU + 0 + j * 4);
+  }
+  if (i0 + 4 < e) {
+    uint2 w = pay[i0 + 4]; scB = s2c[w.x]; lcB = L2[w.y];
+    qB = *(const uint4*)(QK + (size_t)w.y * UU + 0 + j * 4);
+  }
+  for (int i = i0; i < e; i += 4) {
+    uint4 qC = {0, 0, 0, 0}; float scC = 0.f, lcC = 0.f;
+    if (i + 8 < e) {
+      uint2 w = pay[i + 8]; scC = s2c[w.x]; lcC = L2[w.y];
+      qC = *(const uint4*)(QK + (size_t)w.y * UU + 0 + j * 4);
+    }
+    float w = cw2 * __expf(scA - lcA);
+    float qv[8]; unp8(qA, qv);
+#pragma unroll
+    for (int t = 0; t < 8; t++) acc[t] = fmaf(w, qv[t], acc[t]);
+    qA = qB; scA = scB; lcA = lcB;
+    qB = qC; scB = scC; lcB = lcC;
+  }
+#pragma unroll
+  for (int t = 0; t < 8; t++) {
+    float v = acc[t];
+    v += __shfl_xor(v, 16, 64);
+    v += __shfl_xor(v, 32, 64);
+    acc[t] = v;
+  }
+  if (g == 0) *(uint4*)(dAll + (size_t)row * UU + 64 + j * 4) = pk8(acc);
+}
+
+__device__ void dk3_body(int bx, const unsigned* __restrict__ QK,
+                         const float* __restrict__ Tt,
+                         const float* __restrict__ s3c,
+                         const float* __restrict__ L3,
+                         const float* __restrict__ P,
+                         const uint2* __restrict__ pay,
+                         const int* __restrict__ rp,
+                         unsigned* __restrict__ dAll) {
   __shared__ float sT[2 * DD];
   int tid = threadIdx.x;
   sT[tid] = Tt[tid];
   __syncthreads();
-  int row = blockIdx.x * 4 + (tid >> 6);
-  if (row >= NN) return;
+  int row = bx * 4 + (tid >> 6);
   int l = tid & 63, g = l >> 4, j = l & 15;
   float cw3 = P[4];
   int s = rp[row], e = rp[row + 1];
@@ -762,61 +884,21 @@
   if (g == 0) *(uint4*)(dAll + (size_t)row * UU + 192 + j * 4) = pk8(acc);
 }
 
-__global__ __launch_bounds__(256) void em_row(const unsigned* __restrict__ QK,
-                                              const float* __restrict__ Km,
-                                              const float* __restrict__ P,
-                                              unsigned* __restrict__ dAll,
-                                              float* __restrict__ Lm) {
-  __shared__ float sKm[KM * DD];
-  int tid = threadIdx.x;
-  for (int i = tid; i < KM * DD; i += 256) sKm[i] = Km[i];
-  __syncthreads();
-  int row = blockIdx.x * 4 + (tid >> 6);
-  if (row >= NN) return;
-  int l = tid & 63, g = l >> 4, j = l & 15;
-  float bms = P[2] * INV_SQRT_D, cwm = P[5];
-  float q[8];
-  unp8(*(const uint4*)(QK + (size_t)row * UU + 256 + j * 4), q);
-  float dk[8];
-#pragma unroll
-  for (int kk = 0; kk < 8; kk++) {
-    int k = g * 8 + kk;
-    const float* kr = &sKm[k * DD + j * 8];
-    float d = 0.f;
-#pragma unroll
-    for (int t = 0; t < 8; t++) d = fmaf(q[t], kr[t], d);
-    dk[kk] = redsum16(d) * bms;
-  }
-  float m = dk[0];
-#pragma unroll
-  for (int kk = 1; kk < 8; kk++) m = fmaxf(m, dk[kk]);
-  float mx = fmaxf(m, __shfl_xor(m, 16, 64));
-  mx = fmaxf(mx, __shfl_xor(mx, 32, 64));
-  float p[8], z = 0.f;
-#pragma unroll
-  for (int kk = 0; kk < 8; kk++) { p[kk] = __expf(dk[kk] - mx); z += p[kk]; }
-  float zz = z;
-  zz += __shfl_xor(zz, 16, 64);
-  zz += __shfl_xor(zz, 32, 64);
-  if (l == 0) Lm[row] = mx + __logf(zz);
-  float coef = cwm / zz;
-  float acc[8] = {0.f, 0.f, 0.f, 0.f, 0.f, 0.f, 0.f, 0.f};
-#pragma unroll
-  for (int kk = 0; kk < 8; kk++) {
-    int k = g * 8 + kk;
-    const float* kr = &sKm[k * DD + j * 8];
-    float pc_ = p[kk] * coef;
-#pragma unroll
-    for (int t = 0; t < 8; t++) acc[t] = fmaf(pc_, kr[t], acc[t]);
-  }
-#pragma unroll
-  for (int t = 0; t < 8; t++) {
-    float v = acc[t];
-    v += __shfl_xor(v, 16, 64);
-    v += __shfl_xor(v, 32, 64);
-    acc[t] = v;
-  }
-  if (g == 0) *(uint4*)(dAll + (size_t)row * UU + 256 + j * 4) = pk8(acc);
+__global__ __launch_bounds__(256) void phase3_k(const unsigned* __restrict__ QK,
+                                                const float* __restrict__ Tt,
+                                                const float* __restrict__ P,
+                                                const float* __restrict__ s2c,
+                                                const float* __restrict__ L2,
+                                                const uint2* __restrict__ payu2,
+                                                const int* __restrict__ rp_u2,
+                                                const float* __restrict__ s3c,
+                                                const float* __restrict__ L3,
+                                                const uint2* __restrict__ payuv,
+                                                const int* __restrict__ rp_uv,
+                                                unsigned* __restrict__ dAll) {
+  int bx = blockIdx.x;
+  if (bx < ROWB) dk2_body(bx, QK, s2c, L2, P, payu2, rp_u2, dAll);
+  else dk3_body(bx - ROWB, QK, Tt, s3c, L3, P, payuv, rp_uv, dAll);
 }
 
 __global__ __launch_bounds__(256) void ln_bwd(const float* __restrict__ X,
@@ -943,31 +1025,29 @@
 
   params_k<<<1, 64, 0, stream>>>(l2s, l3s, lms, b2s, b3s, bms, Pparams);
 
-  int rowB = (NN + 3) / 4;
-  int mB = (NN + 63) / 64;
+  int rowB = ROWB;
 
   ln_fwd<<<rowB, 256, 0, stream>>>(X, ln_g, ln_b, Gb, meanv, rstdv);
   w_conv<<<320, 256, 0, stream>>>(W_Q2, W_K2, W_Q3, W_K3, W_Qm, Wt5, Wcat);
-  mfma_fwd<<<dim3(mB, 10), 256, 0, stream>>>((const ushort_t*)Gb, Wt5, (ushort_t*)QKall, NN);
   gemm_km<<<1, 256, 0, stream>>>(B_mem, W_Km, Km, KM);
-  edge_mlp<<<EE / 256, 256, 0, stream>>>(EA, We1, be1, We2, be2, a2);
-
-  hist2<<<(EE + 2047) / 2048, 256, 0, stream>>>(c2, u2, cnt_c2, cnt_u2, EE);
-  hist_t3<<<(TT + 2047) / 2048, 256, 0, stream>>>(c3, u3, v3, cnt_c3, cnt_uv, TT);
+  fwd_k<<<MB * 10 + EDGE_BLKS, 256, 0, stream>>>((const ushort_t*)Gb, Wt5, (ushort_t*)QKall,
+                                                 EA, We1, be1, We2, be2, a2);
+
+  hist_k<<<HB2 + HBT, 256, 0, stream>>>(c2, u2, c3, u3, v3, cnt_c2, cnt_u2, cnt_c3, cnt_uv);
   scan_p1<<<dim3(SCAN_NB, 4), 256, 0, stream>>>(cnt, spart);
   scan_p2<<<1, 256, 0, stream>>>(spart);
   scan_p3<<<dim3(SCAN_NB, 4), 256, 0, stream>>>(cnt, spart, rowptr, cursor);
-  scat2<<<(EE + 2047) / 2048, 256, 0, stream>>>(c2, u2, a2, cu_c2, cu_u2, payc2, payu2, EE);
-  scat_t3<<<(TT + 1023) / 1024, 256, 0, stream>>>(c3, u3, v3, ttau, cu_c3, cu_uv,
-                                                  payc3, payuv, TT);
-
-  e2_fused<<<rowB, 256, 0, stream>>>(QKall, Pparams, payc2, rp_c2, s2c, L2, dAll);
-  dk2_gather<<<rowB, 256, 0, stream>>>(QKall, s2c, L2, Pparams, payu2, rp_u2, dAll);
-  t3_fused<<<rowB, 256, 0, stream>>>(QKall, T_tau, Pparams, payc3, rp_c3, s3c, L3, dAll);
-  dk3_gather<<<rowB, 256, 0, stream>>>(QKall, T_tau, s3c, L3, Pparams, payuv, rp_uv, dAll);
-  em_row<<<rowB, 256, 0, stream>>>(QKall, Km, Pparams, dAll, Lm);
-
-  mfma_bwd<<<dim3(mB, 2), 256, 0, stream>>>((const ushort_t*)dAll, Wcat, dG, NN);
+  scat_k<<<HB2 + HBT, 256, 0, stream>>>(c2, u2, a2, cu_c2, cu_u2, payc2, payu2,
+                                        c3, u3, v3, ttau, cu_c3, cu_uv, payc3, payuv);
+
+  phase2_k<<<3 * ROWB, 256, 0, stream>>>(QKall, T_tau, Km, Pparams,
+                                         payc2, rp_c2, payc3, rp_c3,
+                                         s2c, L2, s3c, L3, Lm, dAll);
+  phase3_k<<<2 * ROWB, 256, 0, stream>>>(QKall, T_tau, Pparams,
+                                         s2c, L2, payu2, rp_u2,
+                                         s3c, L3, payuv, rp_uv, dAll);
+
+  mfma_bwd<<<dim3(MB, 2), 256, 0, stream>>>((const ushort_t*)dAll, Wcat, dG, NN);
 
   ln_bwd<<<rowB, 256, 0, stream>>>(X, dG, ln_g, meanv, rstdv, out);
   eval_write<<<(NN + 255) / 256, 256, 0, stream>>>(L2, L3, Lm, Pparams, out + ND);
```

Measured after the change: 949.4 us. +10.2%, slower.
